# Kernel optimization log

Measured on AMD Instinct MI355X. Metric: run time of the kernel, lower is better.

## Reference

```python
import jax, jax.numpy as jnp
import numpy as np

EMBED = 1024
HEADS = 16
HEAD_DIM = EMBED // HEADS
WINDOW = 256  # half-window = 128 on each side
B, S = 2, 2048


def setup_inputs() -> dict:
    key = jax.random.key(0)
    ks = jax.random.split(key, 9)
    std = 1.0 / np.sqrt(EMBED)
    def lin(k):
        kw, kb = jax.random.split(k)
        W = jax.random.uniform(kw, (EMBED, EMBED), jnp.float32, -std, std)
        b = jax.random.uniform(kb, (EMBED,), jnp.float32, -std, std)
        return W, b
    Wq, bq = lin(ks[0])
    Wk, bk = lin(ks[1])
    Wv, bv = lin(ks[2])
    Wo, bo = lin(ks[3])
    x = jax.random.normal(ks[4], (B, S, EMBED), jnp.float32)
    return {"x": x, "Wq": Wq, "bq": bq, "Wk": Wk, "bk": bk,
            "Wv": Wv, "bv": bv, "Wo": Wo, "bo": bo}


def reference(x, Wq, bq, Wk, bk, Wv, bv, Wo, bo):
    b, s, e = x.shape
    h, d = HEADS, HEAD_DIM
    # torch nn.Linear: y = x @ W.T + b
    def proj(W, bias):
        y = jnp.einsum('bse,fe->bsf', x, W) + bias
        return y.reshape(b, s, h, d).transpose(0, 2, 1, 3)  # [b,h,s,d]
    Q = proj(Wq, bq)
    K = proj(Wk, bk)
    V = proj(Wv, bv)
    # local mask: row i attends to cols [i - W//2, i + W//2] inclusive
    idx = jnp.arange(s)
    local_mask = jnp.abs(idx[:, None] - idx[None, :]) <= (WINDOW // 2)  # [s,s] bool
    scores = jnp.einsum('bhqd,bhkd->bhqk', Q, K) / jnp.sqrt(jnp.float32(d))
    scores = jnp.where(local_mask, scores, jnp.float32(-1e9))
    attn = jax.nn.softmax(scores, axis=-1)  # dropout is identity at eval
    out = jnp.einsum('bhqk,bhkd->bhqd', attn, V)
    out = out.transpose(0, 2, 1, 3).reshape(b, s, e)
    output = jnp.einsum('bse,fe->bsf', out, Wo) + bo
    return (output, attn)
```

## Files before the change

### kernel.cpp

```cpp
#include <hip/hip_runtime.h>
#include <hip/hip_bf16.h>
#include <stdint.h>

#define EMBED 1024
#define HEADS 16
#define HDIM 64
#define SEQ 2048
#define BATCH 2
#define MTOT (BATCH*SEQ)
#define KDIM EMBED
#define HALFW 128

typedef __attribute__((ext_vector_type(8))) short short8;
typedef __attribute__((ext_vector_type(4))) float floatx4;

__device__ __forceinline__ ushort f2bf(float f){
  uint32_t x = __float_as_uint(f);
  x += 0x7fffu + ((x >> 16) & 1u);
  return (ushort)(x >> 16);
}

__device__ __forceinline__ void gload16(const ushort* g, ushort* l){
  __builtin_amdgcn_global_load_lds(
      (__attribute__((address_space(1))) void*)(void*)g,
      (__attribute__((address_space(3))) void*)l, 16, 0, 0);
}

__global__ void cast_all(const float* __restrict__ x,  ushort* __restrict__ xb,
                         const float* __restrict__ Wq, const float* __restrict__ Wk,
                         const float* __restrict__ Wv, ushort* __restrict__ wqkv,
                         const float* __restrict__ Wo, ushort* __restrict__ wo)
{
  int bid = blockIdx.x;
  const float* src; ushort* dst; int base;
  if (bid < 4096){ src = x;  dst = xb;   base = bid; }
  else {
    int seg = (bid - 4096) >> 10;
    int sb  = (bid - 4096) & 1023;
    base = sb;
    if      (seg == 0){ src = Wq; dst = wqkv;           }
    else if (seg == 1){ src = Wk; dst = wqkv + 1048576; }
    else if (seg == 2){ src = Wv; dst = wqkv + 2097152; }
    else              { src = Wo; dst = wo;             }
  }
  int i = (base * 256 + threadIdx.x) * 4;
  float4 v = *reinterpret_cast<const float4*>(src + i);
  ushort4 o;
  o.x = f2bf(v.x); o.y = f2bf(v.y); o.z = f2bf(v.z); o.w = f2bf(v.w);
  *reinterpret_cast<ushort4*>(dst + i) = o;
}

__global__ __launch_bounds__(256) void gemm_qkv(
    const ushort* __restrict__ A, const ushort* __restrict__ Bw,
    const float* __restrict__ biasq, const float* __restrict__ biask, const float* __restrict__ biasv,
    ushort* __restrict__ Qo, ushort* __restrict__ Ko, ushort* __restrict__ Vo)
{
  constexpr int BM = 128, BN = 128, BK = 32;
  __shared__ __attribute__((aligned(16))) ushort As[2][BM*BK];
  __shared__ __attribute__((aligned(16))) ushort Bs[2][BN*BK];
  const int tid  = threadIdx.x;
  const int lane = tid & 63;
  const int wid  = tid >> 6;
  const int wr = wid >> 1, wc = wid & 1;

  const int bid = blockIdx.x;
  const int swz = (bid & 7) * 96 + (bid >> 3);
  const int m0 = (swz & 31) * BM;
  const int n0 = (swz >> 5) * BN;

  const int cc0 = tid, cc1 = tid + 256;
  const int row0 = cc0 >> 2, off0 = (cc0 & 3) * 8;
  const int row1 = cc1 >> 2, off1 = (cc1 & 3) * 8;
  const ushort* A0 = A  + (size_t)(m0 + row0) * KDIM + off0;
  const ushort* A1 = A  + (size_t)(m0 + row1) * KDIM + off1;
  const ushort* B0 = Bw + (size_t)(n0 + row0) * KDIM + off0;
  const ushort* B1 = Bw + (size_t)(n0 + row1) * KDIM + off1;

  floatx4 acc[4][4];
  #pragma unroll
  for (int i = 0; i < 4; ++i)
    #pragma unroll
    for (int j = 0; j < 4; ++j) acc[i][j] = (floatx4){0.f, 0.f, 0.f, 0.f};

  const int rsel = lane & 15, ksel = (lane >> 4) * 8;

  gload16(A0, &As[0][cc0 * 8]);
  gload16(B0, &Bs[0][cc0 * 8]);
  gload16(A1, &As[0][cc1 * 8]);
  gload16(B1, &Bs[0][cc1 * 8]);
  __syncthreads();

  int cur = 0;
  for (int kk = 0; kk < KDIM; kk += BK){
    if (kk + BK < KDIM){
      gload16(A0 + kk + BK, &As[cur ^ 1][cc0 * 8]);
      gload16(B0 + kk + BK, &Bs[cur ^ 1][cc0 * 8]);
      gload16(A1 + kk + BK, &As[cur ^ 1][cc1 * 8]);
      gload16(B1 + kk + BK, &Bs[cur ^ 1][cc1 * 8]);
    }
    short8 af[4], bfr[4];
    #pragma unroll
    for (int m = 0; m < 4; ++m)
      af[m] = *reinterpret_cast<const short8*>(&As[cur][(wr*64 + m*16 + rsel) * BK + ksel]);
    #pragma unroll
    for (int n = 0; n < 4; ++n)
      bfr[n] = *reinterpret_cast<const short8*>(&Bs[cur][(wc*64 + n*16 + rsel) * BK + ksel]);
    #pragma unroll
    for (int m = 0; m < 4; ++m)
      #pragma unroll
      for (int n = 0; n < 4; ++n)
        acc[m][n] = __builtin_amdgcn_mfma_f32_16x16x32_bf16(af[m], bfr[n], acc[m][n], 0, 0, 0);
    __syncthreads();
    cur ^= 1;
  }

  const int which = n0 >> 10;
  const float* bias = (which == 0) ? biasq : ((which == 1) ? biask : biasv);
  ushort* dst = (which == 0) ? Qo : ((which == 1) ? Ko : Vo);
  const int nb = n0 & 1023;
  #pragma unroll
  for (int m = 0; m < 4; ++m)
    #pragma unroll
    for (int n = 0; n < 4; ++n)
      #pragma unroll
      for (int r = 0; r < 4; ++r){
        int mg = m0 + wr*64 + m*16 + (lane >> 4)*4 + r;
        int ng = nb + wc*64 + n*16 + (lane & 15);
        float v = acc[m][n][r] + bias[ng];
        int b = mg >> 11, s = mg & (SEQ - 1);
        int h = ng >> 6,  d = ng & 63;
        dst[(((size_t)(b*HEADS + h))*SEQ + s)*HDIM + d] = f2bf(v);
      }
}

__global__ __launch_bounds__(256) void transposeV(const ushort* __restrict__ V,
                                                  ushort* __restrict__ Vt)
{
  __shared__ ushort t[64][72];
  const int tid = threadIdx.x;
  const int bh = blockIdx.y;
  const int s0 = blockIdx.x * 64;
  #pragma unroll
  for (int it = 0; it < 2; ++it){
    int idx = it * 256 + tid;
    int row = idx >> 3, off = (idx & 7) * 8;
    *reinterpret_cast<uint4*>(&t[row][off]) =
        *reinterpret_cast<const uint4*>(V + ((size_t)bh * SEQ + s0 + row) * HDIM + off);
  }
  __syncthreads();
  #pragma unroll
  for (int it = 0; it < 2; ++it){
    int idx = it * 256 + tid;
    int d = idx >> 3, soff = (idx & 7) * 8;
    short8 v;
    #pragma unroll
    for (int e = 0; e < 8; ++e) v[e] = (short)t[soff + e][d];
    *reinterpret_cast<short8*>(Vt + ((size_t)bh * HDIM + d) * SEQ + s0 + soff) = v;
  }
}

__global__ __launch_bounds__(256) void gemm_out(
    const ushort* __restrict__ A, const ushort* __restrict__ Bw,
    const float* __restrict__ bias, float* __restrict__ Co)
{
  constexpr int BM = 64, BN = 128, BK = 32;
  __shared__ __attribute__((aligned(16))) ushort As[2][BM*BK];
  __shared__ __attribute__((aligned(16))) ushort Bs[2][BN*BK];
  const int tid  = threadIdx.x;
  const int lane = tid & 63;
  const int wc   = tid >> 6;

  const int bid = blockIdx.x;
  const int swz = (bid & 7) * 64 + (bid >> 3);
  const int m0 = (swz & 63) * BM;
  const int n0 = (swz >> 6) * BN;

  const int rowA = tid >> 2, offA = (tid & 3) * 8;
  const ushort* Ap  = A  + (size_t)(m0 + rowA) * KDIM + offA;
  const ushort* Bp0 = Bw + (size_t)(n0 + rowA) * KDIM + offA;
  const ushort* Bp1 = Bw + (size_t)(n0 + 64 + rowA) * KDIM + offA;

  floatx4 acc[4][2];
  #pragma unroll
  for (int i = 0; i < 4; ++i)
    #pragma unroll
    for (int j = 0; j < 2; ++j) acc[i][j] = (floatx4){0.f, 0.f, 0.f, 0.f};

  const int rsel = lane & 15, ksel = (lane >> 4) * 8;

  gload16(Ap,  &As[0][tid * 8]);
  gload16(Bp0, &Bs[0][tid * 8]);
  gload16(Bp1, &Bs[0][(tid + 256) * 8]);
  __syncthreads();

  int cur = 0;
  for (int kk = 0; kk < KDIM; kk += BK){
    if (kk + BK < KDIM){
      gload16(Ap  + kk + BK, &As[cur ^ 1][tid * 8]);
      gload16(Bp0 + kk + BK, &Bs[cur ^ 1][tid * 8]);
      gload16(Bp1 + kk + BK, &Bs[cur ^ 1][(tid + 256) * 8]);
    }
    short8 af[4], bfr[2];
    #pragma unroll
    for (int m = 0; m < 4; ++m)
      af[m] = *reinterpret_cast<const short8*>(&As[cur][(m*16 + rsel) * BK + ksel]);
    #pragma unroll
    for (int n = 0; n < 2; ++n)
      bfr[n] = *reinterpret_cast<const short8*>(&Bs[cur][(wc*32 + n*16 + rsel) * BK + ksel]);
    #pragma unroll
    for (int m = 0; m < 4; ++m)
      #pragma unroll
      for (int n = 0; n < 2; ++n)
        acc[m][n] = __builtin_amdgcn_mfma_f32_16x16x32_bf16(af[m], bfr[n], acc[m][n], 0, 0, 0);
    __syncthreads();
    cur ^= 1;
  }

  #pragma unroll
  for (int m = 0; m < 4; ++m)
    #pragma unroll
    for (int n = 0; n < 2; ++n)
      #pragma unroll
      for (int r = 0; r < 4; ++r){
        int mg = m0 + m*16 + (lane >> 4)*4 + r;
        int ng = n0 + wc*32 + n*16 + (lane & 15);
        Co[(size_t)mg * EMBED + ng] = acc[m][n][r] + bias[ng];
      }
}

__global__ __launch_bounds__(256) void attn_kernel(
    const ushort* __restrict__ Qb, const ushort* __restrict__ Kb, const ushort* __restrict__ Vt,
    float* __restrict__ attnp, ushort* __restrict__ ao)
{
  constexpr int TQ = 16;
  constexpr int SPAD = 292;
  constexpr int PPAD = 296;
  __shared__ __attribute__((aligned(16))) float  Ss[TQ][SPAD];
  __shared__ __attribute__((aligned(16))) ushort Pb[TQ][PPAD];
  __shared__ float rowinv[TQ];

  const int tid  = threadIdx.x;
  const int lane = tid & 63;
  const int w    = tid >> 6;
  const int l15  = lane & 15;
  const int lhi  = lane >> 4;
  const int qt = blockIdx.x;
  const int bh = blockIdx.y;
  const int q0 = qt * TQ;
  const int c0 = max(0, q0 - HALFW);
  const int c1 = min(SEQ, q0 + TQ + HALFW);
  const int nc = c1 - c0;
  const int ntiles = nc >> 4;
  const int nks = (nc + 31) >> 5;

  const ushort* Qrow = Qb + ((size_t)bh * SEQ + q0 + l15) * HDIM + lhi * 8;
  const short8 aq0 = *reinterpret_cast<const short8*>(Qrow);
  const short8 aq1 = *reinterpret_cast<const short8*>(Qrow + 32);

  for (int t = w; t < ntiles; t += 4){
    const ushort* Krow = Kb + ((size_t)bh * SEQ + c0 + t*16 + l15) * HDIM + lhi * 8;
    short8 bk0 = *reinterpret_cast<const short8*>(Krow);
    short8 bk1 = *reinterpret_cast<const short8*>(Krow + 32);
    floatx4 acc = (floatx4){0.f, 0.f, 0.f, 0.f};
    acc = __builtin_amdgcn_mfma_f32_16x16x32_bf16(aq0, bk0, acc, 0, 0, 0);
    acc = __builtin_amdgcn_mfma_f32_16x16x32_bf16(aq1, bk1, acc, 0, 0, 0);
    const int c = c0 + t*16 + l15;
    #pragma unroll
    for (int r = 0; r < 4; ++r){
      int q = q0 + lhi*4 + r;
      float s = (c < q - HALFW || c > q + HALFW) ? -1e30f : acc[r] * 0.125f;
      Ss[lhi*4 + r][t*16 + l15] = s;
    }
  }
  __syncthreads();

  const int r  = tid >> 4;
  const int lc = tid & 15;
  float mx = -1e30f;
  for (int j = lc; j < nc; j += 16) mx = fmaxf(mx, Ss[r][j]);
  #pragma unroll
  for (int o = 1; o < 16; o <<= 1) mx = fmaxf(mx, __shfl_xor(mx, o, 64));
  float sum = 0.f;
  for (int j = lc; j < nc; j += 16){
    float p = __expf(Ss[r][j] - mx);
    Ss[r][j] = p;
    Pb[r][j] = f2bf(p);
    sum += p;
  }
  for (int j = nc + lc; j < nks * 32; j += 16) Pb[r][j] = 0;
  #pragma unroll
  for (int o = 1; o < 16; o <<= 1) sum += __shfl_xor(sum, o, 64);
  if (lc == 0) rowinv[r] = 1.f / sum;
  __syncthreads();

  const int jz0 = c0 >> 2, jz1 = c1 >> 2;
  const floatx4 zero4 = (floatx4){0.f, 0.f, 0.f, 0.f};
  for (int rr = 0; rr < TQ; ++rr){
    const float inv = rowinv[rr];
    floatx4* dst = reinterpret_cast<floatx4*>(attnp + ((size_t)bh * SEQ + (q0 + rr)) * SEQ);
    #pragma unroll
    for (int it = 0; it < SEQ / 4 / 256; ++it){
      int j4 = it * 256 + tid;
      floatx4 v = zero4;
      if (j4 >= jz0 && j4 < jz1){
        floatx4 p = *reinterpret_cast<const floatx4*>(&Ss[rr][j4 * 4 - c0]);
        v = (floatx4){p[0] * inv, p[1] * inv, p[2] * inv, p[3] * inv};
      }
      __builtin_nontemporal_store(v, &dst[j4]);
    }
  }

  floatx4 oacc = (floatx4){0.f, 0.f, 0.f, 0.f};
  const ushort* Vrow = Vt + ((size_t)bh * HDIM + w*16 + l15) * SEQ + c0 + lhi * 8;
  for (int ks = 0; ks < nks; ++ks){
    short8 ap = *reinterpret_cast<const short8*>(&Pb[l15][ks*32 + lhi*8]);
    short8 bv = *reinterpret_cast<const short8*>(Vrow + ks*32);
    oacc = __builtin_amdgcn_mfma_f32_16x16x32_bf16(ap, bv, oacc, 0, 0, 0);
  }
  const int b = bh >> 4, h = bh & 15;
  #pragma unroll
  for (int rr = 0; rr < 4; ++rr){
    int q = q0 + lhi*4 + rr;
    float val = oacc[rr] * rowinv[lhi*4 + rr];
    ao[((size_t)(b * SEQ + q)) * EMBED + h * HDIM + w*16 + l15] = f2bf(val);
  }
}

extern "C" void kernel_launch(void* const* d_in, const int* in_sizes, int n_in,
                              void* d_out, int out_size, void* d_ws, size_t ws_size,
                              hipStream_t stream)
{
  const float* x  = (const float*)d_in[0];
  const float* Wq = (const float*)d_in[1];
  const float* bq = (const float*)d_in[2];
  const float* Wk = (const float*)d_in[3];
  const float* bk = (const float*)d_in[4];
  const float* Wv = (const float*)d_in[5];
  const float* bv = (const float*)d_in[6];
  const float* Wo = (const float*)d_in[7];
  const float* bo = (const float*)d_in[8];

  char* ws = (char*)d_ws;
  ushort* xb   = (ushort*)(ws);
  ushort* wqkv = (ushort*)(ws + 8388608);
  ushort* wo   = (ushort*)(ws + 14680064);
  ushort* Qb   = (ushort*)(ws + 16777216);
  ushort* Kb   = (ushort*)(ws + 25165824);
  ushort* Vb   = (ushort*)(ws + 33554432);
  ushort* ao   = (ushort*)(ws + 41943040);
  ushort* Vt   = (ushort*)(ws);

  float* outp  = (float*)d_out;
  float* attnp = outp + (size_t)MTOT * EMBED;

  cast_all<<<8192, 256, 0, stream>>>(x, xb, Wq, Wk, Wv, wqkv, Wo, wo);
  gemm_qkv<<<768, 256, 0, stream>>>(xb, wqkv, bq, bk, bv, Qb, Kb, Vb);
  transposeV<<<dim3(32, 32), 256, 0, stream>>>(Vb, Vt);
  attn_kernel<<<dim3(128, 32), 256, 0, stream>>>(Qb, Kb, Vt, attnp, ao);
  gemm_out<<<512, 256, 0, stream>>>(ao, wo, bo, outp);
}
```

Measured before the change: 186.2 us.

## Enlarge QKV GEMM tile to 128x256x64 and drop LDS double buffering

The QKV projection GEMM now uses 128x256 output tiles with a K-step of 64, and each wave covers all 128 rows by 64 columns. The aim is more reuse of each LDS fragment and fewer loop iterations and barriers. The double-buffered prefetch is replaced by a single buffer that is loaded and then consumed, so global loads no longer overlap MFMA work. The grid is halved to 384 blocks, and each thread now holds 128 accumulator registers, which may lower occupancy on a 256-CU part.

New measurement: 220.5 us. +18.5%, slower.

```diff
diff --git a/kernel.cpp b/kernel.cpp
--- a/kernel.cpp
+++ b/kernel.cpp
@@ -55,63 +55,57 @@
     const float* __restrict__ biasq, const float* __restrict__ biask, const float* __restrict__ biasv,
     ushort* __restrict__ Qo, ushort* __restrict__ Ko, ushort* __restrict__ Vo)
 {
-  constexpr int BM = 128, BN = 128, BK = 32;
-  __shared__ __attribute__((aligned(16))) ushort As[2][BM*BK];
-  __shared__ __attribute__((aligned(16))) ushort Bs[2][BN*BK];
+  constexpr int BM = 128, BN = 256, BK = 64;
+  __shared__ __attribute__((aligned(16))) ushort As[BM*BK];
+  __shared__ __attribute__((aligned(16))) ushort Bs[BN*BK];
   const int tid  = threadIdx.x;
   const int lane = tid & 63;
-  const int wid  = tid >> 6;
-  const int wr = wid >> 1, wc = wid & 1;
+  const int wn   = tid >> 6;
+  const int l15  = lane & 15;
+  const int lhi  = lane >> 4;
 
   const int bid = blockIdx.x;
-  const int swz = (bid & 7) * 96 + (bid >> 3);
+  const int swz = (bid & 7) * 48 + (bid >> 3);
   const int m0 = (swz & 31) * BM;
   const int n0 = (swz >> 5) * BN;
 
-  const int cc0 = tid, cc1 = tid + 256;
-  const int row0 = cc0 >> 2, off0 = (cc0 & 3) * 8;
-  const int row1 = cc1 >> 2, off1 = (cc1 & 3) * 8;
-  const ushort* A0 = A  + (size_t)(m0 + row0) * KDIM + off0;
-  const ushort* A1 = A  + (size_t)(m0 + row1) * KDIM + off1;
-  const ushort* B0 = Bw + (size_t)(n0 + row0) * KDIM + off0;
-  const ushort* B1 = Bw + (size_t)(n0 + row1) * KDIM + off1;
-
-  floatx4 acc[4][4];
-  #pragma unroll
-  for (int i = 0; i < 4; ++i)
+  floatx4 acc[8][4];
+  #pragma unroll
+  for (int i = 0; i < 8; ++i)
     #pragma unroll
     for (int j = 0; j < 4; ++j) acc[i][j] = (floatx4){0.f, 0.f, 0.f, 0.f};
 
-  const int rsel = lane & 15, ksel = (lane >> 4) * 8;
-
-  gload16(A0, &As[0][cc0 * 8]);
-  gload16(B0, &Bs[0][cc0 * 8]);
-  gload16(A1, &As[0][cc1 * 8]);
-  gload16(B1, &Bs[0][cc1 * 8]);
-  __syncthreads();
-
-  int cur = 0;
-  for (int kk = 0; kk < KDIM; kk += BK){
-    if (kk + BK < KDIM){
-      gload16(A0 + kk + BK, &As[cur ^ 1][cc0 * 8]);
-      gload16(B0 + kk + BK, &Bs[cur ^ 1][cc0 * 8]);
-      gload16(A1 + kk + BK, &As[cur ^ 1][cc1 * 8]);
-      gload16(B1 + kk + BK, &Bs[cur ^ 1][cc1 * 8]);
-    }
-    short8 af[4], bfr[4];
-    #pragma unroll
-    for (int m = 0; m < 4; ++m)
-      af[m] = *reinterpret_cast<const short8*>(&As[cur][(wr*64 + m*16 + rsel) * BK + ksel]);
-    #pragma unroll
-    for (int n = 0; n < 4; ++n)
-      bfr[n] = *reinterpret_cast<const short8*>(&Bs[cur][(wc*64 + n*16 + rsel) * BK + ksel]);
-    #pragma unroll
-    for (int m = 0; m < 4; ++m)
-      #pragma unroll
-      for (int n = 0; n < 4; ++n)
-        acc[m][n] = __builtin_amdgcn_mfma_f32_16x16x32_bf16(af[m], bfr[n], acc[m][n], 0, 0, 0);
+  for (int kt = 0; kt < KDIM / BK; ++kt){
+    const int kk = kt * BK;
+    if (kt) __syncthreads();
+    #pragma unroll
+    for (int i = 0; i < 4; ++i){
+      int c = tid + 256 * i;
+      gload16(A + (size_t)(m0 + (c >> 3)) * KDIM + kk + (c & 7) * 8, &As[c * 8]);
+    }
+    #pragma unroll
+    for (int i = 0; i < 8; ++i){
+      int c = tid + 256 * i;
+      gload16(Bw + (size_t)(n0 + (c >> 3)) * KDIM + kk + (c & 7) * 8, &Bs[c * 8]);
+    }
     __syncthreads();
-    cur ^= 1;
+
+    #pragma unroll
+    for (int ksl = 0; ksl < 2; ++ksl){
+      const int ko = ksl * 32 + lhi * 8;
+      short8 af[8], bf[4];
+      #pragma unroll
+      for (int rt = 0; rt < 8; ++rt)
+        af[rt] = *reinterpret_cast<const short8*>(&As[(rt*16 + l15) * BK + ko]);
+      #pragma unroll
+      for (int ct = 0; ct < 4; ++ct)
+        bf[ct] = *reinterpret_cast<const short8*>(&Bs[(wn*64 + ct*16 + l15) * BK + ko]);
+      #pragma unroll
+      for (int rt = 0; rt < 8; ++rt)
+        #pragma unroll
+        for (int ct = 0; ct < 4; ++ct)
+          acc[rt][ct] = __builtin_amdgcn_mfma_f32_16x16x32_bf16(af[rt], bf[ct], acc[rt][ct], 0, 0, 0);
+    }
   }
 
   const int which = n0 >> 10;
@@ -119,14 +113,14 @@
   ushort* dst = (which == 0) ? Qo : ((which == 1) ? Ko : Vo);
   const int nb = n0 & 1023;
   #pragma unroll
-  for (int m = 0; m < 4; ++m)
-    #pragma unroll
-    for (int n = 0; n < 4; ++n)
+  for (int rt = 0; rt < 8; ++rt)
+    #pragma unroll
+    for (int ct = 0; ct < 4; ++ct)
       #pragma unroll
       for (int r = 0; r < 4; ++r){
-        int mg = m0 + wr*64 + m*16 + (lane >> 4)*4 + r;
-        int ng = nb + wc*64 + n*16 + (lane & 15);
-        float v = acc[m][n][r] + bias[ng];
+        int mg = m0 + rt*16 + lhi*4 + r;
+        int ng = nb + wn*64 + ct*16 + l15;
+        float v = acc[rt][ct][r] + bias[ng];
         int b = mg >> 11, s = mg & (SEQ - 1);
         int h = ng >> 6,  d = ng & 63;
         dst[(((size_t)(b*HEADS + h))*SEQ + s)*HDIM + d] = f2bf(v);
@@ -354,7 +348,7 @@
   float* attnp = outp + (size_t)MTOT * EMBED;
 
   cast_all<<<8192, 256, 0, stream>>>(x, xb, Wq, Wk, Wv, wqkv, Wo, wo);
-  gemm_qkv<<<768, 256, 0, stream>>>(xb, wqkv, bq, bk, bv, Qb, Kb, Vb);
+  gemm_qkv<<<384, 256, 0, stream>>>(xb, wqkv, bq, bk, bv, Qb, Kb, Vb);
   transposeV<<<dim3(32, 32), 256, 0, stream>>>(Vb, Vt);
   attn_kernel<<<dim3(128, 32), 256, 0, stream>>>(Qb, Kb, Vt, attnp, ao);
   gemm_out<<<512, 256, 0, stream>>>(ao, wo, bo, outp);
```
